# Kernel tuning notes

Measured on AMD Instinct MI355X. Metric: run time of the kernel, lower is better.

Reference implementation:

```python
import jax, jax.numpy as jnp
import numpy as np

DIM = 512
HID = 2048
BLOCKS = 4
VOCAB = 32000
HEADS = 8
HD = DIM // HEADS
B = 4
T = 257
MBS = 64
LR = 3e-4
EPS = 1e-5


def setup_inputs() -> dict:
    key = jax.random.key(0)
    ks = jax.random.split(key, 10)
    s = 0.02
    n = lambda k, shp: jax.random.normal(k, shp, dtype=jnp.float32) * s
    return {
        'x': jax.random.randint(ks[0], (B, T), 0, VOCAB),
        'embed': n(ks[1], (VOCAB, DIM)),
        'pos': n(ks[2], (MBS, DIM)),
        'ln1_g': jnp.ones((BLOCKS, DIM), jnp.float32),
        'ln1_b': jnp.zeros((BLOCKS, DIM), jnp.float32),
        'qkv_w': n(ks[3], (BLOCKS, DIM, 3 * DIM)),
        'qkv_b': jnp.zeros((BLOCKS, 3 * DIM), jnp.float32),
        'proj_w': n(ks[4], (BLOCKS, DIM, DIM)),
        'proj_b': jnp.zeros((BLOCKS, DIM), jnp.float32),
        'ln2_g': jnp.ones((BLOCKS, DIM), jnp.float32),
        'ln2_b': jnp.zeros((BLOCKS, DIM), jnp.float32),
        'mlp_w1': n(ks[5], (BLOCKS, DIM, HID)),
        'mlp_b1': jnp.zeros((BLOCKS, HID), jnp.float32),
        'mlp_w2': n(ks[6], (BLOCKS, HID, DIM)),
        'mlp_b2': jnp.zeros((BLOCKS, DIM), jnp.float32),
        'lnf_g': jnp.ones((DIM,), jnp.float32),
        'lnf_b': jnp.zeros((DIM,), jnp.float32),
        'head_w': n(ks[7], (DIM, VOCAB)),
        'head_b': jnp.zeros((VOCAB,), jnp.float32),
    }


def _ln(x, g, b):
    m = x.mean(-1, keepdims=True)
    v = ((x - m) ** 2).mean(-1, keepdims=True)
    return (x - m) * jax.lax.rsqrt(v + EPS) * g + b


def _transformer(tokens, static, dyn):
    (embed, pos, ln1_g, ln1_b, qkv_w, qkv_b, proj_w, proj_b,
     ln2_g, ln2_b, lnf_g, lnf_b, head_w, head_b) = static
    mw1, mb1, mw2, mb2 = dyn
    Bx, L = tokens.shape
    h = embed[tokens] + pos[:L]                      # [B, L, D]
    mask = jnp.tril(jnp.ones((L, L), dtype=bool))
    for i in range(BLOCKS):
        xn = _ln(h, ln1_g[i], ln1_b[i])
        qkv = xn @ qkv_w[i] + qkv_b[i]               # [B, L, 3D]
        q, k, v = jnp.split(qkv, 3, axis=-1)
        hd = lambda t: t.reshape(Bx, L, HEADS, HD).transpose(0, 2, 1, 3)
        q, k, v = hd(q), hd(k), hd(v)                # [B, H, L, Dh]
        s = jnp.einsum('bhqd,bhkd->bhqk', q, k) / np.float32(np.sqrt(HD))
        s = jnp.where(mask, s, jnp.float32(-1e9))
        a = jax.nn.softmax(s, axis=-1)
        o = jnp.einsum('bhqk,bhkd->bhqd', a, v).transpose(0, 2, 1, 3).reshape(Bx, L, DIM)
        h = h + o @ proj_w[i] + proj_b[i]
        xn2 = _ln(h, ln2_g[i], ln2_b[i])
        h = h + jax.nn.gelu(xn2 @ mw1[i] + mb1[i]) @ mw2[i] + mb2[i]
    h = _ln(h, lnf_g, lnf_b)
    return h @ head_w + head_b                       # [B, L, V]


def reference(x, embed, pos, ln1_g, ln1_b, qkv_w, qkv_b, proj_w, proj_b,
              ln2_g, ln2_b, mlp_w1, mlp_b1, mlp_w2, mlp_b2,
              lnf_g, lnf_b, head_w, head_b):
    static = (embed, pos, ln1_g, ln1_b, qkv_w, qkv_b, proj_w, proj_b,
              ln2_g, ln2_b, lnf_g, lnf_b, head_w, head_b)
    dyn0 = (mlp_w1, mlp_b1, mlp_w2, mlp_b2)
    n_chunks = (T - 1) // MBS
    inp = x[:, :T - 1].reshape(B, n_chunks, MBS).transpose(1, 0, 2)  # [C, B, b]
    tgt = x[:, 1:T].reshape(B, n_chunks, MBS).transpose(1, 0, 2)

    def step(dyn, chunk):
        ci, ct = chunk
        def loss_fn(d):
            logits = _transformer(ci, static, d)
            logp = jax.nn.log_softmax(logits, axis=-1)
            nll = -jnp.take_along_axis(logp, ct[..., None], axis=-1).squeeze(-1).mean()
            return nll, logits
        grads, logits = jax.grad(loss_fn, has_aux=True)(dyn)
        new_dyn = jax.tree_util.tree_map(lambda p, g: p - LR * g, dyn, grads)
        return new_dyn, logits

    _, logit_chunks = jax.lax.scan(step, dyn0, (inp, tgt))   # [C, B, b, V]
    return logit_chunks.transpose(1, 0, 2, 3).reshape(B, (T - 1), VOCAB)
```

## Files before the change

kernel.cpp:

```cpp
#include <hip/hip_runtime.h>
#include <cstddef>

#define LRATE 3e-4f

typedef short short8 __attribute__((ext_vector_type(8)));
typedef float f32x4 __attribute__((ext_vector_type(4)));
typedef __bf16 bf16x8 __attribute__((ext_vector_type(8)));

__device__ __forceinline__ unsigned short f2b(float f){
  unsigned u = __builtin_bit_cast(unsigned, f);
  unsigned r = (u + 0x7fffu + ((u>>16)&1u)) >> 16;
  return (unsigned short)r;
}
__device__ __forceinline__ float b2f(unsigned short s){
  unsigned u = ((unsigned)s)<<16;
  return __builtin_bit_cast(float, u);
}
__device__ __forceinline__ float gelu_f(float x){
  float u = 0.7978845608028654f*(x + 0.044715f*x*x*x);
  float t = tanhf(u);
  return 0.5f*x*(1.f+t);
}
__device__ __forceinline__ float gelu_df(float x){
  float x2 = x*x;
// ... 414 lines not shown
  int tid = threadIdx.x;
  #pragma unroll
  for(int q=0;q<16;q++){
    int e = tid + q*256;
    int r = e>>6, cc = e&63;
    float v = src[zoff + (size_t)(r0+r)*C + c0+cc];
    unsigned short bvu = f2b(v);
    T[cc*72 + r] = (short)bvu;
    if(dstO) dstO[zoff + (size_t)(r0+r)*C + c0+cc] = bvu;
    if(dstF) dstF[zoff + (size_t)(r0+r)*C + c0+cc] = v;
  }
  __syncthreads();
  #pragma unroll
  for(int q=0;q<2;q++){
    int id = tid*2+q;
    int cc = id>>3, ch = id&7;
    short8 vv = *(const short8*)(T + cc*72 + ch*8);
    *(short8*)(dstT + zoff + (size_t)(c0+cc)*R + r0 + ch*8) = vv;
  }
}

__global__ __launch_bounds__(256) void k_setup(float* stats, float* B1c, const float* b1,
    float* B2c, const float* b2)
{
  int i = blockIdx.x*256 + threadIdx.x;
  if(i < 18432) stats[i] = 0.f;
  if(i < 8192)  B1c[i] = b1[i];
  if(i < 2048)  B2c[i] = b2[i];
}

__global__ __launch_bounds__(256) void k_embed(const int* __restrict__ x, const float* __restrict__ emb,
    const float* __restrict__ pos, float* __restrict__ h, float* __restrict__ S1, float* __restrict__ S2, int chunk)
{
  int n = blockIdx.x, tid = threadIdx.x;
  int b = n>>6, t = n&63;
  int tok = x[b*257 + chunk*64 + t];
  size_t b0 = (size_t)n*512 + tid;
  float v0 = emb[(size_t)tok*512 + tid]       + pos[t*512 + tid];
  float v1 = emb[(size_t)tok*512 + tid + 256] + pos[t*512 + tid + 256];
  h[b0] = v0; h[b0+256] = v1;
  __shared__ float r1[256], r2[256];
  r1[tid] = v0+v1; r2[tid] = v0*v0+v1*v1;
  __syncthreads();
  for(int o=128;o;o>>=1){ if(tid<o){ r1[tid]+=r1[tid+o]; r2[tid]+=r2[tid+o]; } __syncthreads(); }
  if(tid==0){ S1[n]=r1[0]; S2[n]=r2[0]; }
}

__global__ __launch_bounds__(256) void k_ln_bwd(const float* __restrict__ dy, const float* __restrict__ dp, int nz,
    const float* __restrict__ x, const float* __restrict__ g,
    const float* __restrict__ S1v, const float* __restrict__ S2v,
    const float* __restrict__ addin, float* __restrict__ dx, unsigned short* __restrict__ dxb)
{
  int n = blockIdx.x, tid = threadIdx.x;
  float s1 = S1v[n], s2 = S2v[n];
  float m = s1*(1.f/512.f);
  float r = rsqrtf(s2*(1.f/512.f) - m*m + 1e-5f);
  size_t b0 = (size_t)n*512 + tid;
  float dy0, dy1;
  if(nz){
    dy0=0.f; dy1=0.f;
    for(int z=0;z<nz;z++){ dy0 += dp[(size_t)z*131072 + b0]; dy1 += dp[(size_t)z*131072 + b0 + 256]; }
  } else { dy0 = dy[b0]; dy1 = dy[b0+256]; }
  float x0 = x[b0], x1 = x[b0+256];
  float xh0 = (x0-m)*r, xh1 = (x1-m)*r;
  float gh0 = dy0*g[tid], gh1 = dy1*g[tid+256];
  __shared__ float r1[256], r2[256];
  r1[tid] = gh0+gh1; r2[tid] = gh0*xh0 + gh1*xh1;
  __syncthreads();
  for(int o=128;o;o>>=1){ if(tid<o){ r1[tid]+=r1[tid+o]; r2[tid]+=r2[tid+o]; } __syncthreads(); }
  float mg = r1[0]*(1.f/512.f), mgx = r2[0]*(1.f/512.f);
  float d0 = (gh0 - mg - xh0*mgx)*r;
  float d1 = (gh1 - mg - xh1*mgx)*r;
  if(addin){ d0 += addin[b0]; d1 += addin[b0+256]; }
  dx[b0] = d0; dx[b0+256] = d1;
  dxb[b0] = f2b(d0); dxb[b0+256] = f2b(d1);
}

__global__ __launch_bounds__(256) void k_qkv_attn(
    const float* __restrict__ h0, const float* __restrict__ S1, const float* __restrict__ S2,
    const float* __restrict__ lng, const float* __restrict__ lnb,
    const unsigned short* __restrict__ wT, const float* __restrict__ bias,
    unsigned short* __restrict__ qkB, unsigned short* __restrict__ obuf, unsigned short* __restrict__ ap)
{
  __shared__ __align__(16) short Afull[32768];
  __shared__ __align__(16) short Bsl[6*4096];
  __shared__ __align__(16) short Qs[4096], Ks2[4096], Vt[4096];
  short* Pb = Afull;
  float* Sf = (float*)(Afull + 8192);
  int hh=blockIdx.x, bb=blockIdx.y;
  int tid=threadIdx.x, lane=tid&63, w=tid>>6;
  int wr=w>>1, wc=w&1, r16=lane&15, kg=lane>>4, rb=lane>>4;

  int id0=w*128+lane, row0=id0>>3, id1=id0+64, row1=id1>>3;
  float m0,r0v,m1,r1v;
  { float a=S1[bb*64+row0], b=S2[bb*64+row0]; m0=a*(1.f/512.f); r0v=rsqrtf(b*(1.f/512.f)-m0*m0+1e-5f); }
  { float a=S1[bb*64+row1], b=S2[bb*64+row1]; m1=a*(1.f/512.f); r1v=rsqrtf(b*(1.f/512.f)-m1*m1+1e-5f); }
  for(int s=0;s<8;s++){
    #pragma unroll
    for(int q=0;q<2;q++){
      int id = q? id1:id0, row = q? row1:row0;
      float mm = q? m1:m0, rr = q? r1v:r0v;
      int gc=(id&7)^(row&7);
      const float* src = h0 + (size_t)(bb*64+row)*512 + s*64 + gc*8;
      float4 v0=*(const float4*)src, v1=*(const float4*)(src+4);
      const float* gp=lng+s*64+gc*8; const float* bp=lnb+s*64+gc*8;
      float4 g0=*(const float4*)gp, g1=*(const float4*)(gp+4);
      float4 c0=*(const float4*)bp, c1=*(const float4*)(bp+4);
      short8 o;
      o[0]=(short)f2b((v0.x-mm)*rr*g0.x+c0.x);
      o[1]=(short)f2b((v0.y-mm)*rr*g0.y+c0.y);
      o[2]=(short)f2b((v0.z-mm)*rr*g0.z+c0.z);
      o[3]=(short)f2b((v0.w-mm)*rr*g0.w+c0.w);
      o[4]=(short)f2b((v1.x-mm)*rr*g1.x+c1.x);
      o[5]=(short)f2b((v1.y-mm)*rr*g1.y+c1.y);
      o[6]=(short)f2b((v1.z-mm)*rr*g1.z+c1.z);
      o[7]=(short)f2b((v1.w-mm)*rr*g1.w+c1.w);
      *(short8*)((char*)(Afull + s*4096) + id*16) = o;
    }
  }
  __syncthreads();

  for(int p=0;p<3;p++){
    const unsigned short* Bg = wT + (size_t)(p*512 + hh*64)*512;
    auto STB=[&](int t,int slot){
      #pragma unroll
      for(int q=0;q<2;q++){
        int id=w*128+q*64+lane, row=id>>3, gc=(id&7)^(row&7);
        gll16(Bg + (size_t)row*512 + t*64 + gc*8, (char*)Bsl + slot*8192 + id*16);
      }
    };
    #pragma unroll
    for(int s=0;s<4;s++) STB(s,s);
    f32x4 acc[2][2]={};
    for(int t=0;t<8;t++){
      int tt=(t+4<8)? t+4 : 7;
      int slot=(t+4)%6;
      STB(tt, slot);
      asm volatile("s_waitcnt vmcnt(8)" ::: "memory");
      __builtin_amdgcn_sched_barrier(0);
      __builtin_amdgcn_s_barrier();
      __builtin_amdgcn_sched_barrier(0);
      const char* Ab=(const char*)(Afull + t*4096);
      int rslot = (t<6)? t : t-6;
      const char* Bb=(const char*)Bsl + rslot*8192;
      #pragma unroll
      for(int h=0;h<2;h++){
        bf16x8 af[2], bfr[2];
        #pragma unroll
        for(int f=0;f<2;f++){
          int rowa=wr*32+f*16+r16, ca=(h*4+kg)^(rowa&7);
          af[f]=__builtin_bit_cast(bf16x8, *(const short8*)(Ab + rowa*128 + ca*16));
          int rowb=wc*32+f*16+r16, cb=(h*4+kg)^(rowb&7);
          bfr[f]=__builtin_bit_cast(bf16x8, *(const short8*)(Bb + rowb*128 + cb*16));
        }
        #pragma unroll
        for(int fa=0;fa<2;fa++)
          #pragma unroll
          for(int fb=0;fb<2;fb++)
            acc[fa][fb]=__builtin_amdgcn_mfma_f32_16x16x32_bf16(af[fa],bfr[fb],acc[fa][fb],0,0,0);
      }
      asm volatile("s_waitcnt lgkmcnt(0)" ::: "memory");
      __builtin_amdgcn_sched_barrier(0);
    }
    #pragma unroll
    for(int fa=0;fa<2;fa++)
      #pragma unroll
      for(int fb=0;fb<2;fb++)
        #pragma unroll
        for(int i=0;i<4;i++){
          int row=wr*32+fa*16+rb*4+i, col=wc*32+fb*16+r16;
          float v = acc[fa][fb][i] + bias[p*512 + hh*64 + col];
          unsigned short bv16 = f2b(v);
          qkB[(size_t)(bb*64+row)*1536 + p*512 + hh*64 + col] = bv16;
          if(p==0)      tr_write(Qs,  row, col, bv16);
          else if(p==1) tr_write(Ks2, row, col, bv16);
          else          tr_write(Vt,  col, row, bv16);
        }
  }
  __syncthreads();

  f32x4 sa[2][2]={};
  #pragma unroll
  for(int h=0;h<2;h++){
    bf16x8 af[2], bfr[2];
    #pragma unroll
    for(int f=0;f<2;f++){ af[f]=frag_read(Qs, wr*32+f*16+r16, h, kg); bfr[f]=frag_read(Ks2, wc*32+f*16+r16, h, kg); }
    #pragma unroll
    for(int fa=0;fa<2;fa++)
      #pragma unroll
      for(int fb=0;fb<2;fb++)
        sa[fa][fb]=__builtin_amdgcn_mfma_f32_16x16x32_bf16(af[fa],bfr[fb],sa[fa][fb],0,0,0);
  }
  #pragma unroll
  for(int fa=0;fa<2;fa++)
    #pragma unroll
    for(int fb=0;fb<2;fb++)
      #pragma unroll
      for(int i=0;i<4;i++){
        int row=wr*32+fa*16+rb*4+i, col=wc*32+fb*16+r16;
        Sf[row*68+col] = (col<=row) ? sa[fa][fb][i]*0.125f : -1e9f;
      }
  __syncthreads();

  int srow=tid>>2, seg=tid&3;
  float vals[16]; float mx=-3.4e38f;
  #pragma unroll
  for(int k2=0;k2<16;k2++){ vals[k2]=Sf[srow*68+seg*16+k2]; mx=fmaxf(mx,vals[k2]); }
  mx=fmaxf(mx,__shfl_xor(mx,1)); mx=fmaxf(mx,__shfl_xor(mx,2));
  float sm=0;
  #pragma unroll
  for(int k2=0;k2<16;k2++){ vals[k2]=expf(vals[k2]-mx); sm+=vals[k2]; }
  sm+=__shfl_xor(sm,1); sm+=__shfl_xor(sm,2);
  float inv=1.f/sm;
  short8 p0,p1;
  #pragma unroll
  for(int k2=0;k2<8;k2++){ p0[k2]=(short)f2b(vals[k2]*inv); p1[k2]=(short)f2b(vals[k2+8]*inv); }
  __syncthreads();
  *(short8*)((char*)Pb + srow*128 + ((((seg*2)  )^(srow&7))<<4)) = p0;
  *(short8*)((char*)Pb + srow*128 + ((((seg*2+1))^(srow&7))<<4)) = p1;
  unsigned short* apr = ap + ((size_t)(bb*8+hh)*64 + srow)*64 + seg*16;
  *(short8*)apr = p0; *(short8*)(apr+8) = p1;
  __syncthreads();

  f32x4 oa[2][2]={};
  #pragma unroll
  for(int h=0;h<2;h++){
    bf16x8 af[2], bfr[2];
    #pragma unroll
    for(int f=0;f<2;f++){ af[f]=frag_read(Pb, wr*32+f*16+r16, h, kg); bfr[f]=frag_read(Vt, wc*32+f*16+r16, h, kg); }
    #pragma unroll
    for(int fa=0;fa<2;fa++)
      #pragma unroll
      for(int fb=0;fb<2;fb++)
        oa[fa][fb]=__builtin_amdgcn_mfma_f32_16x16x32_bf16(af[fa],bfr[fb],oa[fa][fb],0,0,0);
  }
  #pragma unroll
  for(int fa=0;fa<2;fa++)
    #pragma unroll
    for(int fb=0;fb<2;fb++)
      #pragma unroll
      for(int i=0;i<4;i++){
        int row=wr*32+fa*16+rb*4+i, col=wc*32+fb*16+r16;
        obuf[(size_t)(bb*64+row)*512 + hh*64 + col] = f2b(oa[fa][fb][i]);
      }
}

__global__ __launch_bounds__(256) void k_do_attn(
    const unsigned short* __restrict__ dhBb, const unsigned short* __restrict__ projwB,
    const unsigned short* __restrict__ qkvB, const unsigned short* __restrict__ ap,
    unsigned short* __restrict__ dqkv)
{
  __shared__ __align__(16) short Asm[8192], Bsm2[8192];
  __shared__ __align__(16) short dOs[4096], Vs[4096], Kt[4096], Qt[4096], dOt[4096], Pt[4096], dsN[4096], dsT[4096];
  __shared__ float rsum[64][2];
  int hh=blockIdx.x, bb=blockIdx.y;
  int tid=threadIdx.x, lane=tid&63, w=tid>>6;
  int wr=w>>1, wc=w&1, r16=lane&15, kg=lane>>4, rb=lane>>4;
  const unsigned short* qbase = qkvB + (size_t)bb*64*1536 + hh*64;
  const unsigned short* abase = ap + (size_t)(bb*8+hh)*64*64;

  short8 kreg[2],qreg[2],preg[2];
  #pragma unroll
  for(int q=0;q<2;q++){
    int id=tid*2+q, row=id>>3, c8=id&7;
    kreg[q]=*(const short8*)(qbase+512+(size_t)row*1536+c8*8);
    qreg[q]=*(const short8*)(qbase+(size_t)row*1536+c8*8);
    preg[q]=*(const short8*)(abase+(size_t)row*64+c8*8);
  }
  #pragma unroll
  for(int q=0;q<2;q++){
    int id=w*128+q*64+lane, row=id>>3, gc=(id&7)^(row&7);
    gll16(qbase + 1024 + (size_t)row*1536 + gc*8, (char*)Vs + id*16);
  }

  const unsigned short* Ag = dhBb;
  const unsigned short* Bg = projwB + (size_t)(hh*64)*512;
  auto STAGE=[&](int t,int buf){
    int k0=t*64;
    #pragma unroll
    for(int q=0;q<2;q++){
      int id=w*128+q*64+lane, row=id>>3, gc=(id&7)^(row&7);
      gll16(Ag + (size_t)(bb*64+row)*512 + k0 + gc*8, (char*)(Asm+buf*4096) + id*16);
      gll16(Bg + (size_t)row*512 + k0 + gc*8, (char*)(Bsm2+buf*4096) + id*16);
    }
  };
  STAGE(0,0);
  f32x4 acc[2][2]={};
  for(int t=0;t<8;t++){
    int buf=t&1;
    STAGE(t+1<8?t+1:t, buf^1);
    asm volatile("s_waitcnt vmcnt(4)" ::: "memory");
    __builtin_amdgcn_sched_barrier(0);
    __builtin_amdgcn_s_barrier();
    asm volatile("" ::: "memory");
    const char* Ab=(const char*)(Asm+buf*4096);
    const char* Bb=(const char*)(Bsm2+buf*4096);
    #pragma unroll
    for(int h=0;h<2;h++){
      bf16x8 af[2], bfr[2];
      #pragma unroll
      for(int f=0;f<2;f++){
        int rowa=wr*32+f*16+r16, ca=(h*4+kg)^(rowa&7);
        af[f]=__builtin_bit_cast(bf16x8, *(const short8*)(Ab + rowa*128 + ca*16));
        int rowb=wc*32+f*16+r16, cb=(h*4+kg)^(rowb&7);
        bfr[f]=__builtin_bit_cast(bf16x8, *(const short8*)(Bb + rowb*128 + cb*16));
      }
      #pragma unroll
      for(int fa=0;fa<2;fa++)
        #pragma unroll
        for(int fb=0;fb<2;fb++)
          acc[fa][fb]=__builtin_amdgcn_mfma_f32_16x16x32_bf16(af[fa],bfr[fb],acc[fa][fb],0,0,0);
    }
    asm volatile("s_waitcnt lgkmcnt(0)" ::: "memory");
    __builtin_amdgcn_sched_barrier(0);
    __builtin_amdgcn_s_barrier();
    asm volatile("" ::: "memory");
  }
  #pragma unroll
  for(int fa=0;fa<2;fa++)
    #pragma unroll
    for(int fb=0;fb<2;fb++)
      #pragma unroll
      for(int i=0;i<4;i++){
        int row=wr*32+fa*16+rb*4+i, col=wc*32+fb*16+r16;
        unsigned short db = f2b(acc[fa][fb][i]);
        tr_write(dOs, row, col, db);
        tr_write(dOt, col, row, db);
      }
  #pragma unroll
  for(int q=0;q<2;q++){
    int id=tid*2+q, row=id>>3, c8=id&7;
    #pragma unroll
    for(int j=0;j<8;j++){
      int col=c8*8+j;
      tr_write(Kt, col, row, (unsigned short)kreg[q][j]);
      tr_write(Qt, col, row, (unsigned short)qreg[q][j]);
      tr_write(Pt, col, row, (unsigned short)preg[q][j]);
    }
  }
  asm volatile("s_waitcnt vmcnt(0)" ::: "memory");
  __syncthreads();

  f32x4 da[2][2]={};
  #pragma unroll
  for(int h=0;h<2;h++){
    bf16x8 af[2], bfr[2];
    #pragma unroll
    for(int f=0;f<2;f++){ af[f]=frag_read(dOs, wr*32+f*16+r16, h, kg); bfr[f]=frag_read(Vs, wc*32+f*16+r16, h, kg); }
    #pragma unroll
    for(int fa=0;fa<2;fa++)
      #pragma unroll
      for(int fb=0;fb<2;fb++)
        da[fa][fb]=__builtin_amdgcn_mfma_f32_16x16x32_bf16(af[fa],bfr[fb],da[fa][fb],0,0,0);
  }
  float pv[2][2][4];
  float part[2][4]={};
  #pragma unroll
  for(int fa=0;fa<2;fa++)
    #pragma unroll
    for(int i=0;i<4;i++){
      #pragma unroll
      for(int fb=0;fb<2;fb++){
        int row=wr*32+fa*16+rb*4+i, col=wc*32+fb*16+r16;
        float p = b2f(*(const unsigned short*)((const char*)Pt + col*128 + (((row>>3)^(col&7))<<4) + (row&7)*2));
        pv[fa][fb][i]=p;
        part[fa][i] += p*da[fa][fb][i];
      }
      float s=part[fa][i];
      #pragma unroll
      for(int msk=1;msk<16;msk<<=1) s += __shfl_xor(s,msk);
      part[fa][i]=s;
    }
  if(r16==0){
    #pragma unroll
    for(int fa=0;fa<2;fa++)
      #pragma unroll
      for(int i=0;i<4;i++)
        rsum[wr*32+fa*16+rb*4+i][wc]=part[fa][i];
  }
  __syncthreads();
  #pragma unroll
  for(int fa=0;fa<2;fa++)
    #pragma unroll
    for(int fb=0;fb<2;fb++)
      #pragma unroll
      for(int i=0;i<4;i++){
        int row=wr*32+fa*16+rb*4+i, col=wc*32+fb*16+r16;
        float rt = rsum[row][0]+rsum[row][1];
        float ds = pv[fa][fb][i]*(da[fa][fb][i]-rt)*0.125f;
        unsigned short db = f2b(ds);
        tr_write(dsN, row, col, db);
        tr_write(dsT, col, row, db);
      }
  __syncthreads();

  const short* Amat[3] = {dsN, dsT, Pt};
  const short* Bmat[3] = {Kt,  Qt,  dOt};
  const int ofs[3] = {0, 512, 1024};
  #pragma unroll
  for(int g2=0; g2<3; g2++){
    f32x4 a2[2][2]={};
    #pragma unroll
    for(int h=0;h<2;h++){
      bf16x8 af[2], bfr[2];
      #pragma unroll
      for(int f=0;f<2;f++){ af[f]=frag_read(Amat[g2], wr*32+f*16+r16, h, kg); bfr[f]=frag_read(Bmat[g2], wc*32+f*16+r16, h, kg); }
      #pragma unroll
      for(int fa=0;fa<2;fa++)
        #pragma unroll
        for(int fb=0;fb<2;fb++)
          a2[fa][fb]=__builtin_amdgcn_mfma_f32_16x16x32_bf16(af[fa],bfr[fb],a2[fa][fb],0,0,0);
    }
    #pragma unroll
    for(int fa=0;fa<2;fa++)
      #pragma unroll
      for(int fb=0;fb<2;fb++)
        #pragma unroll
        for(int i=0;i<4;i++){
          int row=wr*32+fa*16+rb*4+i, col=wc*32+fb*16+r16;
          dqkv[(size_t)(bb*64+row)*1536 + hh*64 + ofs[g2] + col] = f2b(a2[fa][fb][i]);
        }
  }
}

__global__ __launch_bounds__(1024) void k_ce_dlog(const float* __restrict__ out, const int* __restrict__ x,
    unsigned short* __restrict__ dlog, int chunk)
{
  __shared__ unsigned short eb[32000];
  __shared__ float red[16];
  int n = blockIdx.x, tid = threadIdx.x;
  int lane = tid&63, w = tid>>6;
  int b = n>>6, t = n&63;
  int R = b*256 + chunk*64 + t;
  int tgt = x[b*257 + chunk*64 + t + 1];
  const float* row = out + (size_t)R*32000;

  float mx = -3.4e38f;
  for(int v=tid; v<32000; v+=1024){ float l=row[v]; mx=fmaxf(mx,l); eb[v]=f2b(l); }
  #pragma unroll
  for(int off=32;off;off>>=1) mx = fmaxf(mx, __shfl_xor(mx,off));
  if(lane==0) red[w]=mx;
  __syncthreads();
  float m = red[0];
  #pragma unroll
  for(int i=1;i<16;i++) m = fmaxf(m, red[i]);
  __syncthreads();

  float s=0;
  for(int v=tid; v<32000; v+=1024){ float e = expf(b2f(eb[v])-m); s+=e; eb[v]=f2b(e); }
  #pragma unroll
  for(int off=32;off;off>>=1) s += __shfl_xor(s,off);
  if(lane==0) red[w]=s;
  __syncthreads();
  float tot = 0.f;
  #pragma unroll
  for(int i=0;i<16;i++) tot += red[i];
  float iz = 1.f/tot * (1.f/256.f);

  unsigned short* dr = dlog + (size_t)n*32000;
  for(int v=tid; v<32000; v+=1024){
    float a = b2f(eb[v])*iz;
    if(v==tgt) a -= (1.f/256.f);
    dr[v] = f2b(a);
  }
}

extern "C" void kernel_launch(void* const* d_in, const int* in_sizes, int n_in,
                              void* d_out, int out_size, void* d_ws, size_t ws_size,
                              hipStream_t stream)
{
  const int*   x      = (const int*)d_in[0];
  const float* embed  = (const float*)d_in[1];
  const float* pos    = (const float*)d_in[2];
// ... 20 lines not shown
  auto AB = [&](size_t bytes)->char*{ char* p = base + off; off += (bytes + 255) & ~(size_t)255; return p; };
  float* W1c  = (float*)AB(16777216);
  float* W2c  = (float*)AB(16777216);
  float* B1c  = (float*)AB(32768);
  float* B2c  = (float*)AB(8192);
  float* hin  = (float*)AB(5*524288);
  float* h1s  = (float*)AB(4*524288);
  float* z1s  = (float*)AB(4*2097152);
  float* dhA  = (float*)AB(524288);
  float* dhB  = (float*)AB(524288);
  float* dxn  = (float*)AB(524288);
  float* dpart= (float*)AB(50*524288);
  float* stats= (float*)AB(4*9*2*256*4);
  unsigned short* qkvwB = (unsigned short*)AB(6291456);
  unsigned short* qkvwT = (unsigned short*)AB(6291456);
  unsigned short* projwB= (unsigned short*)AB(2097152);
  unsigned short* projwT= (unsigned short*)AB(2097152);
  unsigned short* headwB= (unsigned short*)AB(32768000);
  unsigned short* headwT= (unsigned short*)AB(32768000);
  unsigned short* W1b   = (unsigned short*)AB(8388608);
  unsigned short* W1t   = (unsigned short*)AB(8388608);
  unsigned short* W2b   = (unsigned short*)AB(8388608);
  unsigned short* W2t   = (unsigned short*)AB(8388608);
  unsigned short* z1gs  = (unsigned short*)AB(4194304);
  unsigned short* qkBs  = (unsigned short*)AB(4*786432);
  unsigned short* apBs  = (unsigned short*)AB(4*262144);
  unsigned short* obufB = (unsigned short*)AB(262144);
  unsigned short* dlogB = (unsigned short*)AB(16384000);
  unsigned short* dhbB  = (unsigned short*)AB(5*262144);
  unsigned short* dhBb  = (unsigned short*)AB(262144);
  unsigned short* dz1bs = (unsigned short*)AB(4*1048576);
  unsigned short* dqkvB = (unsigned short*)AB(786432);

  auto SS1 = [&](int c, int s)->float*{ return stats + ((size_t)(c*9+s)*2)*256; };
  auto SS2 = [&](int c, int s)->float*{ return stats + ((size_t)(c*9+s)*2)*256 + 256; };

  k_setup<<<72,256,0,stream>>>(stats, B1c, mlp_b1, B2c, mlp_b2);
  k_cvt_t<<<dim3(24,8,4),256,0,stream>>>(qkv_w, qkvwT, qkvwB, nullptr, 512, 1536);
  k_cvt_t<<<dim3(8,8,4),256,0,stream>>>(proj_w, projwT, projwB, nullptr, 512, 512);
  k_cvt_t<<<dim3(500,8,1),256,0,stream>>>(head_w, headwT, headwB, nullptr, 512, 32000);
  k_cvt_t<<<dim3(32,8,4),256,0,stream>>>(mlp_w1, W1t, W1b, W1c, 512, 2048);
  k_cvt_t<<<dim3(8,32,4),256,0,stream>>>(mlp_w2, W2t, W2b, W2c, 2048, 512);

  for(int c=0;c<4;c++){
    k_embed<<<256,256,0,stream>>>(x, embed, pos, hin, SS1(c,0), SS2(c,0), c);
    for(int i=0;i<4;i++){
      float* h0 = hin + (size_t)i*131072;
      float* h2 = hin + (size_t)(i+1)*131072;
      float* h1 = h1s + (size_t)i*131072;
      float* z1 = z1s + (size_t)i*524288;
      unsigned short* z1g = z1gs + (size_t)i*524288;
      unsigned short* qkB = qkBs + (size_t)i*393216;
      unsigned short* apB = apBs + (size_t)i*131072;
      k_qkv_attn<<<dim3(8,4),256,0,stream>>>(h0, SS1(c,i), SS2(c,i), ln1_g+i*512, ln1_b+i*512,
          qkvwT+(size_t)i*786432, qkv_b+i*1536, qkB, obufB, apB);
      k_nt32<0,1><<<dim3(16,8),256,0,stream>>>(obufB, nullptr, nullptr, nullptr, nullptr, nullptr,
          projwT+(size_t)i*262144, proj_b+i*512, h0, nullptr,
          h1, nullptr, SS1(c,5+i), SS2(c,5+i), 256,512,512, 8, 0);
      k_nt32<1,0><<<dim3(64,8),256,0,stream>>>(nullptr, h1, SS1(c,5+i), SS2(c,5+i), ln2_g+i*512, ln2_b+i*512,
          W1t+(size_t)i*1048576, B1c+i*2048, nullptr, nullptr,
          z1, z1g, nullptr, nullptr, 256,2048,512, 8, 1);
      k_nt32<0,1><<<dim3(16,8),256,0,stream>>>(z1g, nullptr, nullptr, nullptr, nullptr, nullptr,
          W2t+(size_t)i*1048576, B2c+i*512, h1, nullptr,
          h2, nullptr, SS1(c,i+1), SS2(c,i+1), 256,512,2048, 32, 0);
    }
    k_nt<128,1,0><<<dim3(250,2),256,0,stream>>>(nullptr, hin+4*131072, SS1(c,4), SS2(c,4), lnf_g, lnf_b,
        headwT, head_b, nullptr, nullptr,
        out, nullptr, nullptr, nullptr, 256,32000,512, 8, 0, c);

    k_ce_dlog<<<256,1024,0,stream>>>(out, x, dlogB, c);
    k_nt<128,0,0><<<dim3(4,2,50),256,0,stream>>>(dlogB, nullptr, nullptr, nullptr, nullptr, nullptr,
        headwB, nullptr, nullptr, nullptr,
        dpart, nullptr, nullptr, nullptr, 256,512,32000, 10, 0, -1);
    k_ln_bwd<<<256,256,0,stream>>>(nullptr, dpart, 50, hin+4*131072, lnf_g, SS1(c,4), SS2(c,4),
        nullptr, dhA, dhbB + 3*131072);
    for(int i=3;i>=0;i--){
      float* h0 = hin + (size_t)i*131072;
      float* h1 = h1s + (size_t)i*131072;
      float* z1 = z1s + (size_t)i*524288;
      unsigned short* qkB = qkBs + (size_t)i*393216;
      unsigned short* apB = apBs + (size_t)i*131072;
      k_nt32<0,0><<<dim3(64,8),256,0,stream>>>(dhbB + (size_t)i*131072, nullptr, nullptr, nullptr, nullptr, nullptr,
          W2b+(size_t)i*1048576, nullptr, nullptr, z1,
          nullptr, dz1bs + (size_t)i*524288, nullptr, nullptr, 256,2048,512, 8, 0);
      k_nt32<0,0><<<dim3(16,8),256,0,stream>>>(dz1bs + (size_t)i*524288, nullptr, nullptr, nullptr, nullptr, nullptr,
          W1b+(size_t)i*1048576, nullptr, nullptr, nullptr,
          dxn, nullptr, nullptr, nullptr, 256,512,2048, 32, 0);
      k_ln_bwd<<<256,256,0,stream>>>(dxn, nullptr, 0, h1, ln2_g+i*512, SS1(c,5+i), SS2(c,5+i),
          dhA, dhB, dhBb);
      k_do_attn<<<dim3(8,4),256,0,stream>>>(dhBb, projwB+(size_t)i*262144, qkB, apB, dqkvB);
      k_nt32<0,0><<<dim3(16,8),256,0,stream>>>(dqkvB, nullptr, nullptr, nullptr, nullptr, nullptr,
          qkvwB+(size_t)i*786432, nullptr, nullptr, nullptr,
          dxn, nullptr, nullptr, nullptr, 256,512,1536, 24, 0);
      k_ln_bwd<<<256,256,0,stream>>>(dxn, nullptr, 0, h0, ln1_g+i*512, SS1(c,i), SS2(c,i),
          dhB, dhA, dhbB + (size_t)((i==0)?4:i-1)*131072);
    }
    k_sgd_all<<<2048,256,0,stream>>>(z1gs, dhbB, dz1bs, h1s, stats, c,
        W1c, W1b, W1t, B1c, W2c, W2b, W2t, B2c, ln2_g, ln2_b);
  }
}
```

Baseline: 2.487 ms.

## Widen attention kernels to 512 threads and use wave shuffles in LN backward

The fused QKV+attention forward and attention backward kernels now run with 8 waves instead of 4. The forward kernel fuses the three Q/K/V projections into one wide N=192 tile with a 3-stage ring. The backward kernel splits the K reduction across two wave groups, computes dV concurrently with dS, and splits dQ/dK between the groups. LN backward replaces its shared-memory tree reduction with wavefront shuffles and a single barrier. Both attention kernels launch only 32 blocks, so this targets latency from low occupancy, at the cost of more barriers and a shared-memory partial-sum reduction.

```diff
diff --git a/kernel.cpp b/kernel.cpp
--- a/kernel.cpp
+++ b/kernel.cpp
@@ -490,6 +490,7 @@
     const float* __restrict__ addin, float* __restrict__ dx, unsigned short* __restrict__ dxb)
 {
   int n = blockIdx.x, tid = threadIdx.x;
+  int lane = tid&63, w4 = tid>>6;
   float s1 = S1v[n], s2 = S2v[n];
   float m = s1*(1.f/512.f);
   float r = rsqrtf(s2*(1.f/512.f) - m*m + 1e-5f);
@@ -502,11 +503,14 @@
   float x0 = x[b0], x1 = x[b0+256];
   float xh0 = (x0-m)*r, xh1 = (x1-m)*r;
   float gh0 = dy0*g[tid], gh1 = dy1*g[tid+256];
-  __shared__ float r1[256], r2[256];
-  r1[tid] = gh0+gh1; r2[tid] = gh0*xh0 + gh1*xh1;
-  __syncthreads();
-  for(int o=128;o;o>>=1){ if(tid<o){ r1[tid]+=r1[tid+o]; r2[tid]+=r2[tid+o]; } __syncthreads(); }
-  float mg = r1[0]*(1.f/512.f), mgx = r2[0]*(1.f/512.f);
+  float a1 = gh0+gh1, a2 = gh0*xh0 + gh1*xh1;
+  #pragma unroll
+  for(int off=32;off;off>>=1){ a1 += __shfl_xor(a1,off); a2 += __shfl_xor(a2,off); }
+  __shared__ float rw[8];
+  if(lane==0){ rw[w4]=a1; rw[4+w4]=a2; }
+  __syncthreads();
+  float mg  = (rw[0]+rw[1]+rw[2]+rw[3])*(1.f/512.f);
+  float mgx = (rw[4]+rw[5]+rw[6]+rw[7])*(1.f/512.f);
   float d0 = (gh0 - mg - xh0*mgx)*r;
   float d1 = (gh1 - mg - xh1*mgx)*r;
   if(addin){ d0 += addin[b0]; d1 += addin[b0+256]; }
@@ -514,34 +518,31 @@
   dxb[b0] = f2b(d0); dxb[b0+256] = f2b(d1);
 }
 
-__global__ __launch_bounds__(256) void k_qkv_attn(
+__global__ __launch_bounds__(512) void k_qkv_attn(
     const float* __restrict__ h0, const float* __restrict__ S1, const float* __restrict__ S2,
     const float* __restrict__ lng, const float* __restrict__ lnb,
     const unsigned short* __restrict__ wT, const float* __restrict__ bias,
     unsigned short* __restrict__ qkB, unsigned short* __restrict__ obuf, unsigned short* __restrict__ ap)
 {
   __shared__ __align__(16) short Afull[32768];
-  __shared__ __align__(16) short Bsl[6*4096];
-  __shared__ __align__(16) short Qs[4096], Ks2[4096], Vt[4096];
-  short* Pb = Afull;
-  float* Sf = (float*)(Afull + 8192);
+  __shared__ __align__(16) short Bsl[3*12288];
+  short* Qs  = Bsl;
+  short* Ks2 = Bsl + 4096;
+  short* Vt  = Bsl + 8192;
+  short* Pb  = Afull;
+  float* Sf  = (float*)(Afull + 8192);
   int hh=blockIdx.x, bb=blockIdx.y;
   int tid=threadIdx.x, lane=tid&63, w=tid>>6;
-  int wr=w>>1, wc=w&1, r16=lane&15, kg=lane>>4, rb=lane>>4;
-
-  int id0=w*128+lane, row0=id0>>3, id1=id0+64, row1=id1>>3;
-  float m0,r0v,m1,r1v;
-  { float a=S1[bb*64+row0], b=S2[bb*64+row0]; m0=a*(1.f/512.f); r0v=rsqrtf(b*(1.f/512.f)-m0*m0+1e-5f); }
-  { float a=S1[bb*64+row1], b=S2[bb*64+row1]; m1=a*(1.f/512.f); r1v=rsqrtf(b*(1.f/512.f)-m1*m1+1e-5f); }
-  for(int s=0;s<8;s++){
-    #pragma unroll
-    for(int q=0;q<2;q++){
-      int id = q? id1:id0, row = q? row1:row0;
-      float mm = q? m1:m0, rr = q? r1v:r0v;
-      int gc=(id&7)^(row&7);
-      const float* src = h0 + (size_t)(bb*64+row)*512 + s*64 + gc*8;
+  int r16=lane&15, kg=lane>>4, rb=lane>>4;
+
+  {
+    int arow=tid>>3, as8=tid&7, agc=as8^(arow&7);
+    float mm,rr;
+    { float a=S1[bb*64+arow], b2=S2[bb*64+arow]; mm=a*(1.f/512.f); rr=rsqrtf(b2*(1.f/512.f)-mm*mm+1e-5f); }
+    for(int s=0;s<8;s++){
+      const float* src = h0 + (size_t)(bb*64+arow)*512 + s*64 + agc*8;
       float4 v0=*(const float4*)src, v1=*(const float4*)(src+4);
-      const float* gp=lng+s*64+gc*8; const float* bp=lnb+s*64+gc*8;
+      const float* gp=lng+s*64+agc*8; const float* bp=lnb+s*64+agc*8;
       float4 g0=*(const float4*)gp, g1=*(const float4*)(gp+4);
       float4 c0=*(const float4*)bp, c1=*(const float4*)(bp+4);
       short8 o;
@@ -553,186 +554,191 @@
       o[5]=(short)f2b((v1.y-mm)*rr*g1.y+c1.y);
       o[6]=(short)f2b((v1.z-mm)*rr*g1.z+c1.z);
       o[7]=(short)f2b((v1.w-mm)*rr*g1.w+c1.w);
-      *(short8*)((char*)(Afull + s*4096) + id*16) = o;
-    }
-  }
-  __syncthreads();
-
-  for(int p=0;p<3;p++){
-    const unsigned short* Bg = wT + (size_t)(p*512 + hh*64)*512;
-    auto STB=[&](int t,int slot){
-      #pragma unroll
-      for(int q=0;q<2;q++){
-        int id=w*128+q*64+lane, row=id>>3, gc=(id&7)^(row&7);
-        gll16(Bg + (size_t)row*512 + t*64 + gc*8, (char*)Bsl + slot*8192 + id*16);
-      }
-    };
-    #pragma unroll
-    for(int s=0;s<4;s++) STB(s,s);
-    f32x4 acc[2][2]={};
-    for(int t=0;t<8;t++){
-      int tt=(t+4<8)? t+4 : 7;
-      int slot=(t+4)%6;
-      STB(tt, slot);
-      asm volatile("s_waitcnt vmcnt(8)" ::: "memory");
-      __builtin_amdgcn_sched_barrier(0);
-      __builtin_amdgcn_s_barrier();
-      __builtin_amdgcn_sched_barrier(0);
-      const char* Ab=(const char*)(Afull + t*4096);
-      int rslot = (t<6)? t : t-6;
-      const char* Bb=(const char*)Bsl + rslot*8192;
-      #pragma unroll
-      for(int h=0;h<2;h++){
-        bf16x8 af[2], bfr[2];
-        #pragma unroll
-        for(int f=0;f<2;f++){
-          int rowa=wr*32+f*16+r16, ca=(h*4+kg)^(rowa&7);
-          af[f]=__builtin_bit_cast(bf16x8, *(const short8*)(Ab + rowa*128 + ca*16));
-          int rowb=wc*32+f*16+r16, cb=(h*4+kg)^(rowb&7);
-          bfr[f]=__builtin_bit_cast(bf16x8, *(const short8*)(Bb + rowb*128 + cb*16));
-        }
-        #pragma unroll
-        for(int fa=0;fa<2;fa++)
-          #pragma unroll
-          for(int fb=0;fb<2;fb++)
-            acc[fa][fb]=__builtin_amdgcn_mfma_f32_16x16x32_bf16(af[fa],bfr[fb],acc[fa][fb],0,0,0);
-      }
-      asm volatile("s_waitcnt lgkmcnt(0)" ::: "memory");
-      __builtin_amdgcn_sched_barrier(0);
-    }
-    #pragma unroll
-    for(int fa=0;fa<2;fa++)
-      #pragma unroll
-      for(int fb=0;fb<2;fb++)
-        #pragma unroll
-        for(int i=0;i<4;i++){
-          int row=wr*32+fa*16+rb*4+i, col=wc*32+fb*16+r16;
-          float v = acc[fa][fb][i] + bias[p*512 + hh*64 + col];
-          unsigned short bv16 = f2b(v);
-          qkB[(size_t)(bb*64+row)*1536 + p*512 + hh*64 + col] = bv16;
-          if(p==0)      tr_write(Qs,  row, col, bv16);
-          else if(p==1) tr_write(Ks2, row, col, bv16);
-          else          tr_write(Vt,  col, row, bv16);
-        }
-  }
-  __syncthreads();
-
-  f32x4 sa[2][2]={};
+      *(short8*)((char*)(Afull) + s*8192 + tid*16) = o;
+    }
+  }
+  __syncthreads();
+
+  auto STB=[&](int t,int slot){
+    #pragma unroll
+    for(int q=0;q<3;q++){
+      int cid=q*512+tid, brow=cid>>3, s8=cid&7, gc=s8^(brow&7);
+      int p=brow>>6, cin=brow&63;
+      gll16(wT + (size_t)(p*512+hh*64+cin)*512 + t*64 + gc*8, (char*)Bsl + slot*24576 + cid*16);
+    }
+  };
+  STB(0,0); STB(1,1);
+  int wr=w>>2, wc=w&3;
+  f32x4 acc[2][3]={};
+  for(int t=0;t<8;t++){
+    int tt=(t+2<8)? t+2 : 7;
+    STB(tt,(t+2)%3);
+    asm volatile("s_waitcnt vmcnt(6)" ::: "memory");
+    __builtin_amdgcn_sched_barrier(0);
+    __builtin_amdgcn_s_barrier();
+    __builtin_amdgcn_sched_barrier(0);
+    const char* Ab=(const char*)Afull + t*8192;
+    const char* Bb=(const char*)Bsl + (t%3)*24576;
+    #pragma unroll
+    for(int h=0;h<2;h++){
+      bf16x8 af[2], bfr[3];
+      #pragma unroll
+      for(int fa=0;fa<2;fa++){
+        int rowa=wr*32+fa*16+r16, ca=(h*4+kg)^(rowa&7);
+        af[fa]=__builtin_bit_cast(bf16x8, *(const short8*)(Ab + rowa*128 + ca*16));
+      }
+      #pragma unroll
+      for(int fb=0;fb<3;fb++){
+        int rowb=wc*48+fb*16+r16, cb=(h*4+kg)^(rowb&7);
+        bfr[fb]=__builtin_bit_cast(bf16x8, *(const short8*)(Bb + rowb*128 + cb*16));
+      }
+      #pragma unroll
+      for(int fa=0;fa<2;fa++)
+        #pragma unroll
+        for(int fb=0;fb<3;fb++)
+          acc[fa][fb]=__builtin_amdgcn_mfma_f32_16x16x32_bf16(af[fa],bfr[fb],acc[fa][fb],0,0,0);
+    }
+    asm volatile("s_waitcnt lgkmcnt(0)" ::: "memory");
+    __builtin_amdgcn_sched_barrier(0);
+    __builtin_amdgcn_s_barrier();
+    __builtin_amdgcn_sched_barrier(0);
+  }
+  asm volatile("s_waitcnt vmcnt(0)" ::: "memory");
+  __syncthreads();
+
+  #pragma unroll
+  for(int fa=0;fa<2;fa++)
+    #pragma unroll
+    for(int fb=0;fb<3;fb++)
+      #pragma unroll
+      for(int i=0;i<4;i++){
+        int row=wr*32+fa*16+rb*4+i;
+        int band=wc*3+fb;
+        int p=band>>2, cin=(band&3)*16+r16;
+        float v = acc[fa][fb][i] + bias[p*512 + hh*64 + cin];
+        unsigned short bv16 = f2b(v);
+        qkB[(size_t)(bb*64+row)*1536 + p*512 + hh*64 + cin] = bv16;
+        if(p==0)      tr_write(Qs,  row, cin, bv16);
+        else if(p==1) tr_write(Ks2, row, cin, bv16);
+        else          tr_write(Vt,  cin, row, bv16);
+      }
+  __syncthreads();
+
+  int wr2=w>>2, wc2=w&3;
+  f32x4 sa[2]={};
   #pragma unroll
   for(int h=0;h<2;h++){
-    bf16x8 af[2], bfr[2];
-    #pragma unroll
-    for(int f=0;f<2;f++){ af[f]=frag_read(Qs, wr*32+f*16+r16, h, kg); bfr[f]=frag_read(Ks2, wc*32+f*16+r16, h, kg); }
-    #pragma unroll
-    for(int fa=0;fa<2;fa++)
-      #pragma unroll
-      for(int fb=0;fb<2;fb++)
-        sa[fa][fb]=__builtin_amdgcn_mfma_f32_16x16x32_bf16(af[fa],bfr[fb],sa[fa][fb],0,0,0);
+    bf16x8 bfr = frag_read(Ks2, wc2*16+r16, h, kg);
+    #pragma unroll
+    for(int fa=0;fa<2;fa++){
+      bf16x8 af = frag_read(Qs, wr2*32+fa*16+r16, h, kg);
+      sa[fa]=__builtin_amdgcn_mfma_f32_16x16x32_bf16(af,bfr,sa[fa],0,0,0);
+    }
   }
   #pragma unroll
   for(int fa=0;fa<2;fa++)
     #pragma unroll
-    for(int fb=0;fb<2;fb++)
-      #pragma unroll
-      for(int i=0;i<4;i++){
-        int row=wr*32+fa*16+rb*4+i, col=wc*32+fb*16+r16;
-        Sf[row*68+col] = (col<=row) ? sa[fa][fb][i]*0.125f : -1e9f;
-      }
-  __syncthreads();
-
-  int srow=tid>>2, seg=tid&3;
-  float vals[16]; float mx=-3.4e38f;
-  #pragma unroll
-  for(int k2=0;k2<16;k2++){ vals[k2]=Sf[srow*68+seg*16+k2]; mx=fmaxf(mx,vals[k2]); }
-  mx=fmaxf(mx,__shfl_xor(mx,1)); mx=fmaxf(mx,__shfl_xor(mx,2));
-  float sm=0;
-  #pragma unroll
-  for(int k2=0;k2<16;k2++){ vals[k2]=expf(vals[k2]-mx); sm+=vals[k2]; }
-  sm+=__shfl_xor(sm,1); sm+=__shfl_xor(sm,2);
-  float inv=1.f/sm;
-  short8 p0,p1;
-  #pragma unroll
-  for(int k2=0;k2<8;k2++){ p0[k2]=(short)f2b(vals[k2]*inv); p1[k2]=(short)f2b(vals[k2+8]*inv); }
-  __syncthreads();
-  *(short8*)((char*)Pb + srow*128 + ((((seg*2)  )^(srow&7))<<4)) = p0;
-  *(short8*)((char*)Pb + srow*128 + ((((seg*2+1))^(srow&7))<<4)) = p1;
-  unsigned short* apr = ap + ((size_t)(bb*8+hh)*64 + srow)*64 + seg*16;
-  *(short8*)apr = p0; *(short8*)(apr+8) = p1;
-  __syncthreads();
-
-  f32x4 oa[2][2]={};
+    for(int i=0;i<4;i++){
+      int row=wr2*32+fa*16+rb*4+i, col=wc2*16+r16;
+      Sf[row*68+col] = (col<=row) ? sa[fa][i]*0.125f : -1e9f;
+    }
+  __syncthreads();
+
+  {
+    int srow=tid>>3, seg8=tid&7;
+    float vals[8]; float mx=-3.4e38f;
+    #pragma unroll
+    for(int k2=0;k2<8;k2++){ vals[k2]=Sf[srow*68+seg8*8+k2]; mx=fmaxf(mx,vals[k2]); }
+    mx=fmaxf(mx,__shfl_xor(mx,1)); mx=fmaxf(mx,__shfl_xor(mx,2)); mx=fmaxf(mx,__shfl_xor(mx,4));
+    float sm=0;
+    #pragma unroll
+    for(int k2=0;k2<8;k2++){ vals[k2]=expf(vals[k2]-mx); sm+=vals[k2]; }
+    sm+=__shfl_xor(sm,1); sm+=__shfl_xor(sm,2); sm+=__shfl_xor(sm,4);
+    float inv=1.f/sm;
+    short8 p0;
+    #pragma unroll
+    for(int k2=0;k2<8;k2++) p0[k2]=(short)f2b(vals[k2]*inv);
+    __syncthreads();
+    *(short8*)((char*)Pb + srow*128 + (((seg8)^(srow&7))<<4)) = p0;
+    *(short8*)(ap + ((size_t)(bb*8+hh)*64 + srow)*64 + seg8*8) = p0;
+  }
+  __syncthreads();
+
+  f32x4 oa[2]={};
   #pragma unroll
   for(int h=0;h<2;h++){
-    bf16x8 af[2], bfr[2];
-    #pragma unroll
-    for(int f=0;f<2;f++){ af[f]=frag_read(Pb, wr*32+f*16+r16, h, kg); bfr[f]=frag_read(Vt, wc*32+f*16+r16, h, kg); }
-    #pragma unroll
-    for(int fa=0;fa<2;fa++)
-      #pragma unroll
-      for(int fb=0;fb<2;fb++)
-        oa[fa][fb]=__builtin_amdgcn_mfma_f32_16x16x32_bf16(af[fa],bfr[fb],oa[fa][fb],0,0,0);
+    bf16x8 bfr = frag_read(Vt, wc2*16+r16, h, kg);
+    #pragma unroll
+    for(int fa=0;fa<2;fa++){
+      bf16x8 af = frag_read(Pb, wr2*32+fa*16+r16, h, kg);
+      oa[fa]=__builtin_amdgcn_mfma_f32_16x16x32_bf16(af,bfr,oa[fa],0,0,0);
+    }
   }
   #pragma unroll
   for(int fa=0;fa<2;fa++)
     #pragma unroll
-    for(int fb=0;fb<2;fb++)
-      #pragma unroll
-      for(int i=0;i<4;i++){
-        int row=wr*32+fa*16+rb*4+i, col=wc*32+fb*16+r16;
-        obuf[(size_t)(bb*64+row)*512 + hh*64 + col] = f2b(oa[fa][fb][i]);
-      }
-}
-
-__global__ __launch_bounds__(256) void k_do_attn(
+    for(int i=0;i<4;i++){
+      int row=wr2*32+fa*16+rb*4+i, col=wc2*16+r16;
+      obuf[(size_t)(bb*64+row)*512 + hh*64 + col] = f2b(oa[fa][i]);
+    }
+}
+
+__global__ __launch_bounds__(512) void k_do_attn(
     const unsigned short* __restrict__ dhBb, const unsigned short* __restrict__ projwB,
     const unsigned short* __restrict__ qkvB, const unsigned short* __restrict__ ap,
     unsigned short* __restrict__ dqkv)
 {
-  __shared__ __align__(16) short Asm[8192], Bsm2[8192];
+  __shared__ __align__(16) short Asl[4*4096];
+  __shared__ __align__(16) short Bsl2[4*4096];
   __shared__ __align__(16) short dOs[4096], Vs[4096], Kt[4096], Qt[4096], dOt[4096], Pt[4096], dsN[4096], dsT[4096];
   __shared__ float rsum[64][2];
+  float* Pacc = (float*)Asl;
   int hh=blockIdx.x, bb=blockIdx.y;
   int tid=threadIdx.x, lane=tid&63, w=tid>>6;
-  int wr=w>>1, wc=w&1, r16=lane&15, kg=lane>>4, rb=lane>>4;
+  int wg=w>>2, wl=w&3;
+  int wr=wl>>1, wc=wl&1, r16=lane&15, kg=lane>>4, rb=lane>>4;
   const unsigned short* qbase = qkvB + (size_t)bb*64*1536 + hh*64;
   const unsigned short* abase = ap + (size_t)(bb*8+hh)*64*64;
 
-  short8 kreg[2],qreg[2],preg[2];
-  #pragma unroll
-  for(int q=0;q<2;q++){
-    int id=tid*2+q, row=id>>3, c8=id&7;
-    kreg[q]=*(const short8*)(qbase+512+(size_t)row*1536+c8*8);
-    qreg[q]=*(const short8*)(qbase+(size_t)row*1536+c8*8);
-    preg[q]=*(const short8*)(abase+(size_t)row*64+c8*8);
-  }
-  #pragma unroll
-  for(int q=0;q<2;q++){
-    int id=w*128+q*64+lane, row=id>>3, gc=(id&7)^(row&7);
-    gll16(qbase + 1024 + (size_t)row*1536 + gc*8, (char*)Vs + id*16);
-  }
-
-  const unsigned short* Ag = dhBb;
+  {
+    int row=tid>>3, gc=(tid&7)^(row&7);
+    gll16(qbase + 1024 + (size_t)row*1536 + gc*8, (char*)Vs + tid*16);
+  }
+  {
+    int row=tid>>3, c8=tid&7;
+    short8 kreg=*(const short8*)(qbase+512+(size_t)row*1536+c8*8);
+    short8 qreg=*(const short8*)(qbase+(size_t)row*1536+c8*8);
+    short8 preg=*(const short8*)(abase+(size_t)row*64+c8*8);
+    #pragma unroll
+    for(int j=0;j<8;j++){
+      int col=c8*8+j;
+      tr_write(Kt, col, row, (unsigned short)kreg[j]);
+      tr_write(Qt, col, row, (unsigned short)qreg[j]);
+      tr_write(Pt, col, row, (unsigned short)preg[j]);
+    }
+  }
+
   const unsigned short* Bg = projwB + (size_t)(hh*64)*512;
   auto STAGE=[&](int t,int buf){
-    int k0=t*64;
+    int k0=(wg*4+t)*64;
     #pragma unroll
     for(int q=0;q<2;q++){
-      int id=w*128+q*64+lane, row=id>>3, gc=(id&7)^(row&7);
-      gll16(Ag + (size_t)(bb*64+row)*512 + k0 + gc*8, (char*)(Asm+buf*4096) + id*16);
-      gll16(Bg + (size_t)row*512 + k0 + gc*8, (char*)(Bsm2+buf*4096) + id*16);
+      int id=wl*128+q*64+lane, row=id>>3, gc=(id&7)^(row&7);
+      gll16(dhBb + (size_t)(bb*64+row)*512 + k0 + gc*8, (char*)Asl + (wg*2+buf)*8192 + id*16);
+      gll16(Bg + (size_t)row*512 + k0 + gc*8, (char*)Bsl2 + (wg*2+buf)*8192 + id*16);
     }
   };
   STAGE(0,0);
   f32x4 acc[2][2]={};
-  for(int t=0;t<8;t++){
+  for(int t=0;t<4;t++){
     int buf=t&1;
-    STAGE(t+1<8?t+1:t, buf^1);
+    STAGE(t+1<4?t+1:t, buf^1);
     asm volatile("s_waitcnt vmcnt(4)" ::: "memory");
     __builtin_amdgcn_sched_barrier(0);
     __builtin_amdgcn_s_barrier();
-    asm volatile("" ::: "memory");
-    const char* Ab=(const char*)(Asm+buf*4096);
-    const char* Bb=(const char*)(Bsm2+buf*4096);
+    __builtin_amdgcn_sched_barrier(0);
+    const char* Ab=(const char*)Asl + (wg*2+buf)*8192;
+    const char* Bb=(const char*)Bsl2 + (wg*2+buf)*8192;
     #pragma unroll
     for(int h=0;h<2;h++){
       bf16x8 af[2], bfr[2];
@@ -752,97 +758,121 @@
     asm volatile("s_waitcnt lgkmcnt(0)" ::: "memory");
     __builtin_amdgcn_sched_barrier(0);
     __builtin_amdgcn_s_barrier();
-    asm volatile("" ::: "memory");
-  }
-  #pragma unroll
-  for(int fa=0;fa<2;fa++)
-    #pragma unroll
-    for(int fb=0;fb<2;fb++)
-      #pragma unroll
-      for(int i=0;i<4;i++){
-        int row=wr*32+fa*16+rb*4+i, col=wc*32+fb*16+r16;
-        unsigned short db = f2b(acc[fa][fb][i]);
-        tr_write(dOs, row, col, db);
-        tr_write(dOt, col, row, db);
-      }
-  #pragma unroll
-  for(int q=0;q<2;q++){
-    int id=tid*2+q, row=id>>3, c8=id&7;
-    #pragma unroll
-    for(int j=0;j<8;j++){
-      int col=c8*8+j;
-      tr_write(Kt, col, row, (unsigned short)kreg[q][j]);
-      tr_write(Qt, col, row, (unsigned short)qreg[q][j]);
-      tr_write(Pt, col, row, (unsigned short)preg[q][j]);
-    }
+    __builtin_amdgcn_sched_barrier(0);
   }
   asm volatile("s_waitcnt vmcnt(0)" ::: "memory");
   __syncthreads();
 
+  if(wg==1){
+    #pragma unroll
+    for(int fa=0;fa<2;fa++)
+      #pragma unroll
+      for(int fb=0;fb<2;fb++)
+        #pragma unroll
+        for(int i=0;i<4;i++){
+          int row=wr*32+fa*16+rb*4+i, col=wc*32+fb*16+r16;
+          Pacc[row*64+col]=acc[fa][fb][i];
+        }
+  }
+  __syncthreads();
+  if(wg==0){
+    #pragma unroll
+    for(int fa=0;fa<2;fa++)
+      #pragma unroll
+      for(int fb=0;fb<2;fb++)
+        #pragma unroll
+        for(int i=0;i<4;i++){
+          int row=wr*32+fa*16+rb*4+i, col=wc*32+fb*16+r16;
+          unsigned short db = f2b(acc[fa][fb][i] + Pacc[row*64+col]);
+          tr_write(dOs, row, col, db);
+          tr_write(dOt, col, row, db);
+        }
+  }
+  __syncthreads();
+
   f32x4 da[2][2]={};
-  #pragma unroll
-  for(int h=0;h<2;h++){
-    bf16x8 af[2], bfr[2];
-    #pragma unroll
-    for(int f=0;f<2;f++){ af[f]=frag_read(dOs, wr*32+f*16+r16, h, kg); bfr[f]=frag_read(Vs, wc*32+f*16+r16, h, kg); }
-    #pragma unroll
-    for(int fa=0;fa<2;fa++)
-      #pragma unroll
-      for(int fb=0;fb<2;fb++)
-        da[fa][fb]=__builtin_amdgcn_mfma_f32_16x16x32_bf16(af[fa],bfr[fb],da[fa][fb],0,0,0);
-  }
   float pv[2][2][4];
-  float part[2][4]={};
-  #pragma unroll
-  for(int fa=0;fa<2;fa++)
-    #pragma unroll
-    for(int i=0;i<4;i++){
-      #pragma unroll
-      for(int fb=0;fb<2;fb++){
-        int row=wr*32+fa*16+rb*4+i, col=wc*32+fb*16+r16;
-        float p = b2f(*(const unsigned short*)((const char*)Pt + col*128 + (((row>>3)^(col&7))<<4) + (row&7)*2));
-        pv[fa][fb][i]=p;
-        part[fa][i] += p*da[fa][fb][i];
-      }
-      float s=part[fa][i];
-      #pragma unroll
-      for(int msk=1;msk<16;msk<<=1) s += __shfl_xor(s,msk);
-      part[fa][i]=s;
-    }
-  if(r16==0){
-    #pragma unroll
-    for(int fa=0;fa<2;fa++)
-      #pragma unroll
-      for(int i=0;i<4;i++)
-        rsum[wr*32+fa*16+rb*4+i][wc]=part[fa][i];
-  }
-  __syncthreads();
-  #pragma unroll
-  for(int fa=0;fa<2;fa++)
-    #pragma unroll
-    for(int fb=0;fb<2;fb++)
-      #pragma unroll
-      for(int i=0;i<4;i++){
-        int row=wr*32+fa*16+rb*4+i, col=wc*32+fb*16+r16;
-        float rt = rsum[row][0]+rsum[row][1];
-        float ds = pv[fa][fb][i]*(da[fa][fb][i]-rt)*0.125f;
-        unsigned short db = f2b(ds);
-        tr_write(dsN, row, col, db);
-        tr_write(dsT, col, row, db);
-      }
-  __syncthreads();
-
-  const short* Amat[3] = {dsN, dsT, Pt};
-  const short* Bmat[3] = {Kt,  Qt,  dOt};
-  const int ofs[3] = {0, 512, 1024};
-  #pragma unroll
-  for(int g2=0; g2<3; g2++){
-    f32x4 a2[2][2]={};
+  if(wg==0){
     #pragma unroll
     for(int h=0;h<2;h++){
       bf16x8 af[2], bfr[2];
       #pragma unroll
-      for(int f=0;f<2;f++){ af[f]=frag_read(Amat[g2], wr*32+f*16+r16, h, kg); bfr[f]=frag_read(Bmat[g2], wc*32+f*16+r16, h, kg); }
+      for(int f=0;f<2;f++){ af[f]=frag_read(dOs, wr*32+f*16+r16, h, kg); bfr[f]=frag_read(Vs, wc*32+f*16+r16, h, kg); }
+      #pragma unroll
+      for(int fa=0;fa<2;fa++)
+        #pragma unroll
+        for(int fb=0;fb<2;fb++)
+          da[fa][fb]=__builtin_amdgcn_mfma_f32_16x16x32_bf16(af[fa],bfr[fb],da[fa][fb],0,0,0);
+    }
+    float part[2][4]={};
+    #pragma unroll
+    for(int fa=0;fa<2;fa++)
+      #pragma unroll
+      for(int i=0;i<4;i++){
+        #pragma unroll
+        for(int fb=0;fb<2;fb++){
+          int row=wr*32+fa*16+rb*4+i, col=wc*32+fb*16+r16;
+          float p = b2f(*(const unsigned short*)((const char*)Pt + col*128 + (((row>>3)^(col&7))<<4) + (row&7)*2));
+          pv[fa][fb][i]=p;
+          part[fa][i] += p*da[fa][fb][i];
+        }
+        float s=part[fa][i];
+        #pragma unroll
+        for(int msk=1;msk<16;msk<<=1) s += __shfl_xor(s,msk);
+        if(r16==0) rsum[wr*32+fa*16+rb*4+i][wc]=s;
+      }
+  } else {
+    f32x4 dvv[2][2]={};
+    #pragma unroll
+    for(int h=0;h<2;h++){
+      bf16x8 af[2], bfr[2];
+      #pragma unroll
+      for(int f=0;f<2;f++){ af[f]=frag_read(Pt, wr*32+f*16+r16, h, kg); bfr[f]=frag_read(dOt, wc*32+f*16+r16, h, kg); }
+      #pragma unroll
+      for(int fa=0;fa<2;fa++)
+        #pragma unroll
+        for(int fb=0;fb<2;fb++)
+          dvv[fa][fb]=__builtin_amdgcn_mfma_f32_16x16x32_bf16(af[fa],bfr[fb],dvv[fa][fb],0,0,0);
+    }
+    #pragma unroll
+    for(int fa=0;fa<2;fa++)
+      #pragma unroll
+      for(int fb=0;fb<2;fb++)
+        #pragma unroll
+        for(int i=0;i<4;i++){
+          int row=wr*32+fa*16+rb*4+i, col=wc*32+fb*16+r16;
+          dqkv[(size_t)(bb*64+row)*1536 + hh*64 + 1024 + col] = f2b(dvv[fa][fb][i]);
+        }
+  }
+  __syncthreads();
+
+  if(wg==0){
+    #pragma unroll
+    for(int fa=0;fa<2;fa++)
+      #pragma unroll
+      for(int fb=0;fb<2;fb++)
+        #pragma unroll
+        for(int i=0;i<4;i++){
+          int row=wr*32+fa*16+rb*4+i, col=wc*32+fb*16+r16;
+          float rt = rsum[row][0]+rsum[row][1];
+          float ds = pv[fa][fb][i]*(da[fa][fb][i]-rt)*0.125f;
+          unsigned short db = f2b(ds);
+          tr_write(dsN, row, col, db);
+          tr_write(dsT, col, row, db);
+        }
+  }
+  __syncthreads();
+
+  {
+    const short* Am = wg ? dsT : dsN;
+    const short* Bm = wg ? Qt  : Kt;
+    int ofs = wg ? 512 : 0;
+    f32x4 a2[2][2]={};
+    #pragma unroll
+    for(int h=0;h<2;h++){
+      bf16x8 af[2], bfr[2];
+      #pragma unroll
+      for(int f=0;f<2;f++){ af[f]=frag_read(Am, wr*32+f*16+r16, h, kg); bfr[f]=frag_read(Bm, wc*32+f*16+r16, h, kg); }
       #pragma unroll
       for(int fa=0;fa<2;fa++)
         #pragma unroll
@@ -856,7 +886,7 @@
         #pragma unroll
         for(int i=0;i<4;i++){
           int row=wr*32+fa*16+rb*4+i, col=wc*32+fb*16+r16;
-          dqkv[(size_t)(bb*64+row)*1536 + hh*64 + ofs[g2] + col] = f2b(a2[fa][fb][i]);
+          dqkv[(size_t)(bb*64+row)*1536 + hh*64 + ofs + col] = f2b(a2[fa][fb][i]);
         }
   }
 }
@@ -983,7 +1013,7 @@
       unsigned short* z1g = z1gs + (size_t)i*524288;
       unsigned short* qkB = qkBs + (size_t)i*393216;
       unsigned short* apB = apBs + (size_t)i*131072;
-      k_qkv_attn<<<dim3(8,4),256,0,stream>>>(h0, SS1(c,i), SS2(c,i), ln1_g+i*512, ln1_b+i*512,
+      k_qkv_attn<<<dim3(8,4),512,0,stream>>>(h0, SS1(c,i), SS2(c,i), ln1_g+i*512, ln1_b+i*512,
           qkvwT+(size_t)i*786432, qkv_b+i*1536, qkB, obufB, apB);
       k_nt32<0,1><<<dim3(16,8),256,0,stream>>>(obufB, nullptr, nullptr, nullptr, nullptr, nullptr,
           projwT+(size_t)i*262144, proj_b+i*512, h0, nullptr,
@@ -1019,7 +1049,7 @@
           dxn, nullptr, nullptr, nullptr, 256,512,2048, 32, 0);
       k_ln_bwd<<<256,256,0,stream>>>(dxn, nullptr, 0, h1, ln2_g+i*512, SS1(c,5+i), SS2(c,5+i),
           dhA, dhB, dhBb);
-      k_do_attn<<<dim3(8,4),256,0,stream>>>(dhBb, projwB+(size_t)i*262144, qkB, apB, dqkvB);
+      k_do_attn<<<dim3(8,4),512,0,stream>>>(dhBb, projwB+(size_t)i*262144, qkB, apB, dqkvB);
       k_nt32<0,0><<<dim3(16,8),256,0,stream>>>(dqkvB, nullptr, nullptr, nullptr, nullptr, nullptr,
           qkvwB+(size_t)i*786432, nullptr, nullptr, nullptr,
           dxn, nullptr, nullptr, nullptr, 256,512,1536, 24, 0);
```

Result: faster. 2.364 ms (-4.9%).
